# Optimization experiments

Hardware: AMD Instinct MI355X
Metric: run time of the kernel (lower is better)

Reference implementation:

```python
import jax, jax.numpy as jnp
import numpy as np

K = 27          # kernel volume = 3^3 (kernel_size=3, dimension=3)
M = 100000      # active in/out pairs per kernel offset
N_IN = 200000   # input sparse points
N_OUT = 400000  # output sparse points (stride-2 transpose upsample)
C_IN = 32
C_OUT = 32


def setup_inputs() -> dict:
    key = jax.random.key(0)
    k1, k2, k3, k4 = jax.random.split(key, 4)
    feats = jax.random.normal(k1, (N_IN, C_IN), dtype=jnp.float32)
    kernel = jax.random.normal(k2, (K, C_IN, C_OUT), dtype=jnp.float32) * 0.05
    in_map = jax.random.randint(k3, (K, M), 0, N_IN, dtype=jnp.int32)
    out_map = jax.random.randint(k4, (K, M), 0, N_OUT, dtype=jnp.int32)
    return {"feats": feats, "kernel": kernel, "in_map": in_map,
            "out_map": out_map, "n_out": N_OUT}


def reference(feats, kernel, in_map, out_map, n_out):
    # Sparse conv-transpose: for each kernel offset k,
    #   gather input rows, multiply by the offset's weight matrix,
    #   scatter-add into the output coordinate rows.
    gathered = feats[in_map]                              # [K, M, C_in]
    per_off = jnp.einsum('kmc,kcd->kmd', gathered, kernel)  # [K, M, C_out]
    c_out = kernel.shape[-1]
    out = jnp.zeros((n_out, c_out), dtype=feats.dtype)
    out = out.at[out_map.reshape(-1)].add(per_off.reshape(-1, c_out))
    return out
```

## Files before the change

### kernel.cpp

```cpp
#include <hip/hip_runtime.h>

#define KOFF 27
#define MPAIR 100000
#define NPAIR (KOFF * MPAIR)
#define NIN 200000
#define NOUT 400000
#define CIN 32
#define COUT 32

#define ROWS_PER_BIN 256
#define NBIN ((NOUT + ROWS_PER_BIN - 1) / ROWS_PER_BIN)
#define CAPB 3072
#define BPB 8192
#define SPILL_CAP 65536

#define O_SPCNT   ((size_t)8192)
#define O_SPILL   ((size_t)8448)
#define O_BINNED  ((size_t)532736)
#define O_PEROFF  ((size_t)19738880)
#define O_F16     ((size_t)192538880)
#define WS_NEED   ((size_t)205338880)

typedef unsigned int uint4n __attribute__((ext_vector_type(4)));

__device__ __forceinline__ unsigned int bf16pair(float a, float b) {
    unsigned int ua = __float_as_uint(a), ub = __float_as_uint(b);
    ua = (ua + 0x7fffu + ((ua >> 16) & 1u)) >> 16;
    ub = (ub + 0x7fffu + ((ub >> 16) & 1u)) >> 16;
    return ua | (ub << 16);
}
__device__ __forceinline__ float bf2f(unsigned short v) {
    return __uint_as_float(((unsigned int)v) << 16);
}
__device__ __forceinline__ float bf2f_lo(unsigned int w) {
    return __uint_as_float(w << 16);
}
__device__ __forceinline__ float bf2f_hi(unsigned int w) {
    return __uint_as_float(w & 0xFFFF0000u);
}

__global__ __launch_bounds__(256) void cvt_kernel(
    const float* __restrict__ feats, unsigned short* __restrict__ f16)
{
    int i = blockIdx.x * 256 + threadIdx.x;
    if (i >= NIN * CIN / 8) return;
    const float4* src = reinterpret_cast<const float4*>(feats) + i * 2;
    float4 a = src[0], b = src[1];
    uint4n u;
    u.x = bf16pair(a.x, a.y); u.y = bf16pair(a.z, a.w);
    u.z = bf16pair(b.x, b.y); u.w = bf16pair(b.z, b.w);
    reinterpret_cast<uint4n*>(f16)[i] = u;
}

__global__ __launch_bounds__(256) void bin_kernel(
    const int* __restrict__ out_map,
    int* __restrict__ gbin, int* __restrict__ binned,
    int* __restrict__ spill_cnt, int2* __restrict__ spill)
{
    __shared__ int lhist[NBIN];
    const int t = threadIdx.x;
    const int base = blockIdx.x * BPB;

    for (int c = t; c < NBIN; c += 256) lhist[c] = 0;
    __syncthreads();

    for (int i = t; i < BPB; i += 256) {
        int p = base + i;
        if (p < NPAIR) atomicAdd(&lhist[out_map[p] >> 8], 1);
    }
    __syncthreads();

    for (int c = t; c < NBIN; c += 256) {
        int cnt = lhist[c];
        lhist[c] = (cnt > 0) ? atomicAdd(&gbin[c], cnt) : 0;
    }
    __syncthreads();

    for (int i = t; i < BPB; i += 256) {
        int p = base + i;
        if (p >= NPAIR) continue;
        int row = out_map[p];
        int bin = row >> 8;
        int val = ((row & 255) << 22) | p;
        int pos = atomicAdd(&lhist[bin], 1);
        if (pos < CAPB) {
            binned[(size_t)bin * CAPB + pos] = val;
        } else {
            int o = atomicAdd(spill_cnt, 1);
            if (o < SPILL_CAP) spill[o] = make_int2(row, p);
        }
    }
}

__global__ __launch_bounds__(256) void mv_kernel(
    const unsigned short* __restrict__ f16, const float* __restrict__ weight,
    const int* __restrict__ in_map, unsigned short* __restrict__ per_off)
{
    const int k = blockIdx.y;
    const int m = blockIdx.x * 256 + threadIdx.x;
    if (m >= MPAIR) return;
    const int p = k * MPAIR + m;
    const int in_row = in_map[p];

    const uint4n* frow = reinterpret_cast<const uint4n*>(f16 + (size_t)in_row * CIN);
    uint4n q[2];
    q[0] = frow[0]; q[1] = frow[1];

    float f[CIN];
#pragma unroll
    for (int j = 0; j < 2; ++j) {
        f[j*16 + 0]  = bf2f_lo(q[j].x); f[j*16 + 1]  = bf2f_hi(q[j].x);
        f[j*16 + 2]  = bf2f_lo(q[j].y); f[j*16 + 3]  = bf2f_hi(q[j].y);
        f[j*16 + 4]  = bf2f_lo(q[j].z); f[j*16 + 5]  = bf2f_hi(q[j].z);
        f[j*16 + 6]  = bf2f_lo(q[j].w); f[j*16 + 7]  = bf2f_hi(q[j].w);
    }
    uint4n q2[2];
    q2[0] = frow[2]; q2[1] = frow[3];
#pragma unroll
    for (int j = 0; j < 2; ++j) {
        f[16 + j*8 + 0] = bf2f_lo(q2[j].x); f[16 + j*8 + 1] = bf2f_hi(q2[j].x);
        f[16 + j*8 + 2] = bf2f_lo(q2[j].y); f[16 + j*8 + 3] = bf2f_hi(q2[j].y);
        f[16 + j*8 + 4] = bf2f_lo(q2[j].z); f[16 + j*8 + 5] = bf2f_hi(q2[j].z);
        f[16 + j*8 + 6] = bf2f_lo(q2[j].w); f[16 + j*8 + 7] = bf2f_hi(q2[j].w);
    }
#pragma unroll
    for (int j = 0; j < 2; ++j) {
        f[j*8 + 0] = bf2f_lo(q[j].x); f[j*8 + 1] = bf2f_hi(q[j].x);
        f[j*8 + 2] = bf2f_lo(q[j].y); f[j*8 + 3] = bf2f_hi(q[j].y);
        f[j*8 + 4] = bf2f_lo(q[j].z); f[j*8 + 5] = bf2f_hi(q[j].z);
        f[j*8 + 6] = bf2f_lo(q[j].w); f[j*8 + 7] = bf2f_hi(q[j].w);
    }

    float acc[COUT];
#pragma unroll
    for (int i = 0; i < COUT; ++i) acc[i] = 0.f;

    const float* wk = weight + (size_t)k * (CIN * COUT);
#pragma unroll
    for (int ci = 0; ci < CIN; ++ci) {
        const float fv = f[ci];
#pragma unroll
        for (int co = 0; co < COUT; ++co)
            acc[co] = fmaf(fv, wk[ci * COUT + co], acc[co]);
    }

    uint4n u[4];
#pragma unroll
    for (int j = 0; j < 4; ++j) {
        u[j].x = bf16pair(acc[8 * j + 0], acc[8 * j + 1]);
        u[j].y = bf16pair(acc[8 * j + 2], acc[8 * j + 3]);
        u[j].z = bf16pair(acc[8 * j + 4], acc[8 * j + 5]);
        u[j].w = bf16pair(acc[8 * j + 6], acc[8 * j + 7]);
    }
    uint4n* dst = reinterpret_cast<uint4n*>(per_off + (size_t)p * COUT);
#pragma unroll
    for (int j = 0; j < 4; ++j) dst[j] = u[j];
}

__global__ __launch_bounds__(256) void gather3_kernel(
    const unsigned short* __restrict__ per_off,
    const int* __restrict__ gbin, const int* __restrict__ binned,
    float* __restrict__ out)
{
    __shared__ int sorted[CAPB];
    __shared__ int cnt[ROWS_PER_BIN];
    __shared__ int scn[ROWS_PER_BIN];
    __shared__ int cur[ROWS_PER_BIN];

    const int bin = blockIdx.x;
    const int t = threadIdx.x;
    const int n = min(gbin[bin], CAPB);
    const int* mybin = binned + (size_t)bin * CAPB;

    cnt[t] = 0;
    __syncthreads();

    for (int i = t; i < n; i += 256)
        atomicAdd(&cnt[(mybin[i] >> 22) & 255], 1);
    __syncthreads();

    scn[t] = cnt[t];
    __syncthreads();
#pragma unroll
    for (int off = 1; off < 256; off <<= 1) {
        int v = (t >= off) ? scn[t - off] : 0;
        __syncthreads();
        scn[t] += v;
        __syncthreads();
    }
    cur[t] = scn[t] - cnt[t];
    __syncthreads();

    for (int i = t; i < n; i += 256) {
        int v = mybin[i];
        int pos = atomicAdd(&cur[(v >> 22) & 255], 1);
        sorted[pos] = v & 0x3FFFFF;
    }
    __syncthreads();

    const int g = t >> 5, lane = t & 31;
    for (int r = g; r < ROWS_PER_BIN; r += 8) {
        int grow = (bin << 8) + r;
        if (grow >= NOUT) break;
        int s1 = scn[r], s0 = s1 - cnt[r];
        float a0 = 0.f, a1 = 0.f, a2 = 0.f, a3 = 0.f;
        int i = s0;
        for (; i + 4 <= s1; i += 4) {
            int p0 = sorted[i], p1 = sorted[i + 1], p2 = sorted[i + 2], p3 = sorted[i + 3];
            a0 += bf2f(per_off[(size_t)p0 * COUT + lane]);
            a1 += bf2f(per_off[(size_t)p1 * COUT + lane]);
            a2 += bf2f(per_off[(size_t)p2 * COUT + lane]);
            a3 += bf2f(per_off[(size_t)p3 * COUT + lane]);
        }
        for (; i < s1; ++i)
            a0 += bf2f(per_off[(size_t)sorted[i] * COUT + lane]);
        out[(size_t)grow * COUT + lane] = (a0 + a1) + (a2 + a3);
    }
}

__global__ __launch_bounds__(256) void spill_kernel(
    const float* __restrict__ feats, const float* __restrict__ weight,
    const int* __restrict__ in_map,
    const int* __restrict__ spill_cnt, const int2* __restrict__ spill,
    float* __restrict__ out)
{
    int n = min(*spill_cnt, SPILL_CAP);
    for (int i = blockIdx.x * blockDim.x + threadIdx.x; i < n * 32;
         i += gridDim.x * blockDim.x) {
        int idx = i >> 5, co = i & 31;
        int2 s = spill[idx];
        int row = s.x;
        int p   = s.y;
        int k   = p / MPAIR;
        int irow = in_map[p];
        const float* f  = feats + (size_t)irow * CIN;
        const float* wk = weight + (size_t)k * (CIN * COUT);
        float acc = 0.f;
#pragma unroll
        for (int ci = 0; ci < CIN; ++ci)
            acc = fmaf(f[ci], wk[ci * COUT + co], acc);
        atomicAdd(&out[(size_t)row * COUT + co], acc);
    }
}

__global__ __launch_bounds__(256) void spconvt_fallback(
    const float* __restrict__ feats, const float* __restrict__ weight,
    const int* __restrict__ in_map, const int* __restrict__ out_map,
    float* __restrict__ out)
{
    const int k = blockIdx.y;
    const int m = blockIdx.x * blockDim.x + threadIdx.x;
    const bool active = (m < MPAIR);
    const int mm = active ? m : (MPAIR - 1);
    const int pair = k * MPAIR + mm;
    const int in_row = in_map[pair];
    const int out_row = out_map[pair];
    const float4* frow = reinterpret_cast<const float4*>(feats + (size_t)in_row * CIN);
    float4 f4[8];
#pragma unroll
    for (int i = 0; i < 8; ++i) f4[i] = frow[i];
    const float* f = reinterpret_cast<const float*>(f4);
    float acc[COUT];
#pragma unroll
    for (int i = 0; i < COUT; ++i) acc[i] = 0.f;
    const float* wk = weight + (size_t)k * (CIN * COUT);
#pragma unroll
    for (int ci = 0; ci < CIN; ++ci) {
        const float fv = f[ci];
#pragma unroll
        for (int co = 0; co < COUT; ++co)
            acc[co] = fmaf(fv, wk[ci * COUT + co], acc[co]);
    }
    if (active) {
        float* orow = out + (size_t)out_row * COUT;
#pragma unroll
        for (int co = 0; co < COUT; ++co) atomicAdd(orow + co, acc[co]);
    }
}

extern "C" void kernel_launch(void* const* d_in, const int* in_sizes, int n_in,
                              void* d_out, int out_size, void* d_ws, size_t ws_size,
                              hipStream_t stream) {
    const float* feats  = (const float*)d_in[0];
    const float* weight = (const float*)d_in[1];
    const int* in_map   = (const int*)d_in[2];
    const int* out_map  = (const int*)d_in[3];
    float* out          = (float*)d_out;
    char* ws            = (char*)d_ws;

    if (ws_size >= WS_NEED) {
        int* gbin               = (int*)(ws);
        int* spill_cnt          = (int*)(ws + O_SPCNT);
        int2* spill             = (int2*)(ws + O_SPILL);
        int* binned             = (int*)(ws + O_BINNED);
        unsigned short* per_off = (unsigned short*)(ws + O_PEROFF);
        unsigned short* f16     = (unsigned short*)(ws + O_F16);

        (void)hipMemsetAsync(ws, 0, O_SPILL, stream);

        cvt_kernel<<<dim3((NIN * CIN / 8 + 255) / 256), dim3(256), 0, stream>>>(
            feats, f16);

        bin_kernel<<<dim3((NPAIR + BPB - 1) / BPB), dim3(256), 0, stream>>>(
            out_map, gbin, binned, spill_cnt, spill);

        mv_kernel<<<dim3((MPAIR + 255) / 256, KOFF), dim3(256), 0, stream>>>(
            f16, weight, in_map, per_off);

        gather3_kernel<<<dim3(NBIN), dim3(256), 0, stream>>>(
            per_off, gbin, binned, out);

        spill_kernel<<<dim3(64), dim3(256), 0, stream>>>(
            feats, weight, in_map, spill_cnt, spill, out);
    } else {
        (void)hipMemsetAsync(d_out, 0, (size_t)out_size * sizeof(float), stream);
        spconvt_fallback<<<dim3((MPAIR + 255) / 256, KOFF), dim3(256), 0, stream>>>(
            feats, weight, in_map, out_map, out);
    }
}
```

Baseline: 297.1 us.

## Counting-sort pairs by input-row chunk so the matvec gathers feats locally

Adds a three-pass counting sort (histogram, scan, scatter) that groups pairs by kernel offset and by 1024-row chunk of the input feature table. The matvec kernel is rewritten to walk each (offset, chunk) bucket, so the bf16 feature gathers hit a small, cache-resident region instead of random rows. This costs three extra passes over in_map plus a binned index buffer, and the per_off stores become scattered writes indexed by the original pair id. Blocks are ordered so the chunks of each offset group run together, which may help L2 reuse.

```diff
diff --git a/kernel.cpp b/kernel.cpp
--- a/kernel.cpp
+++ b/kernel.cpp
@@ -14,12 +14,20 @@
 #define BPB 8192
 #define SPILL_CAP 65536
 
-#define O_SPCNT   ((size_t)8192)
-#define O_SPILL   ((size_t)8448)
-#define O_BINNED  ((size_t)532736)
-#define O_PEROFF  ((size_t)19738880)
-#define O_F16     ((size_t)192538880)
-#define WS_NEED   ((size_t)205338880)
+#define CHROWS 1024
+#define NCHUNK ((NIN + CHROWS - 1) / CHROWS)
+#define NBINC (KOFF * NCHUNK)
+
+#define O_CNTC    ((size_t)8192)
+#define O_SPCNT   ((size_t)32768)
+#define O_SPILL   ((size_t)33024)
+#define O_BASC    ((size_t)560128)
+#define O_CURC    ((size_t)581632)
+#define O_BINNED  ((size_t)603136)
+#define O_BINI    ((size_t)19809280)
+#define O_PEROFF  ((size_t)30609280)
+#define O_F16     ((size_t)203409280)
+#define WS_NEED   ((size_t)216209280)
 
 typedef unsigned int uint4n __attribute__((ext_vector_type(4)));
 
@@ -50,6 +58,84 @@
     u.x = bf16pair(a.x, a.y); u.y = bf16pair(a.z, a.w);
     u.z = bf16pair(b.x, b.y); u.w = bf16pair(b.z, b.w);
     reinterpret_cast<uint4n*>(f16)[i] = u;
+}
+
+__global__ __launch_bounds__(256) void histc_kernel(
+    const int* __restrict__ in_map, int* __restrict__ cntc)
+{
+    __shared__ int h[NBINC];
+    const int t = threadIdx.x;
+    const int base = blockIdx.x * BPB;
+    for (int c = t; c < NBINC; c += 256) h[c] = 0;
+    __syncthreads();
+    for (int i = t; i < BPB; i += 256) {
+        int p = base + i;
+        if (p < NPAIR) {
+            int key = (p / MPAIR) * NCHUNK + (in_map[p] >> 10);
+            atomicAdd(&h[key], 1);
+        }
+    }
+    __syncthreads();
+    for (int c = t; c < NBINC; c += 256) if (h[c]) atomicAdd(&cntc[c], h[c]);
+}
+
+__global__ __launch_bounds__(256) void scanc_kernel(
+    const int* __restrict__ cntc, int* __restrict__ basc, int* __restrict__ curc)
+{
+    __shared__ int lsum[256];
+    const int t = threadIdx.x;
+    int v[21]; int s = 0;
+#pragma unroll
+    for (int j = 0; j < 21; ++j) {
+        int i = t * 21 + j;
+        v[j] = (i < NBINC) ? cntc[i] : 0;
+        s += v[j];
+    }
+    lsum[t] = s;
+    __syncthreads();
+    for (int off = 1; off < 256; off <<= 1) {
+        int w = (t >= off) ? lsum[t - off] : 0;
+        __syncthreads();
+        lsum[t] += w;
+        __syncthreads();
+    }
+    int run = lsum[t] - s;
+#pragma unroll
+    for (int j = 0; j < 21; ++j) {
+        int i = t * 21 + j;
+        if (i < NBINC) { basc[i] = run; curc[i] = run; run += v[j]; }
+    }
+    if (t == 255) basc[NBINC] = run;
+}
+
+__global__ __launch_bounds__(256) void scatc_kernel(
+    const int* __restrict__ in_map, int* __restrict__ curc,
+    unsigned int* __restrict__ binned_in)
+{
+    __shared__ int h[NBINC];
+    const int t = threadIdx.x;
+    const int base = blockIdx.x * BPB;
+    for (int c = t; c < NBINC; c += 256) h[c] = 0;
+    __syncthreads();
+    for (int i = t; i < BPB; i += 256) {
+        int p = base + i;
+        if (p < NPAIR)
+            atomicAdd(&h[(p / MPAIR) * NCHUNK + (in_map[p] >> 10)], 1);
+    }
+    __syncthreads();
+    for (int c = t; c < NBINC; c += 256) {
+        int v = h[c];
+        h[c] = v ? atomicAdd(&curc[c], v) : 0;
+    }
+    __syncthreads();
+    for (int i = t; i < BPB; i += 256) {
+        int p = base + i;
+        if (p >= NPAIR) continue;
+        int ir = in_map[p];
+        int key = (p / MPAIR) * NCHUNK + (ir >> 10);
+        int slot = atomicAdd(&h[key], 1);
+        binned_in[slot] = ((unsigned int)(ir & 1023) << 22) | (unsigned int)p;
+    }
 }
 
 __global__ __launch_bounds__(256) void bin_kernel(
@@ -92,69 +178,77 @@
     }
 }
 
-__global__ __launch_bounds__(256) void mv_kernel(
+__global__ __launch_bounds__(256) void mv3_kernel(
     const unsigned short* __restrict__ f16, const float* __restrict__ weight,
-    const int* __restrict__ in_map, unsigned short* __restrict__ per_off)
-{
-    const int k = blockIdx.y;
-    const int m = blockIdx.x * 256 + threadIdx.x;
-    if (m >= MPAIR) return;
-    const int p = k * MPAIR + m;
-    const int in_row = in_map[p];
-
-    const uint4n* frow = reinterpret_cast<const uint4n*>(f16 + (size_t)in_row * CIN);
-    uint4n q[2];
-    q[0] = frow[0]; q[1] = frow[1];
-
-    float f[CIN];
-#pragma unroll
-    for (int j = 0; j < 2; ++j) {
-        f[j*16 + 0]  = bf2f_lo(q[j].x); f[j*16 + 1]  = bf2f_hi(q[j].x);
-        f[j*16 + 2]  = bf2f_lo(q[j].y); f[j*16 + 3]  = bf2f_hi(q[j].y);
-        f[j*16 + 4]  = bf2f_lo(q[j].z); f[j*16 + 5]  = bf2f_hi(q[j].z);
-        f[j*16 + 6]  = bf2f_lo(q[j].w); f[j*16 + 7]  = bf2f_hi(q[j].w);
-    }
-    uint4n q2[2];
-    q2[0] = frow[2]; q2[1] = frow[3];
-#pragma unroll
-    for (int j = 0; j < 2; ++j) {
-        f[16 + j*8 + 0] = bf2f_lo(q2[j].x); f[16 + j*8 + 1] = bf2f_hi(q2[j].x);
-        f[16 + j*8 + 2] = bf2f_lo(q2[j].y); f[16 + j*8 + 3] = bf2f_hi(q2[j].y);
-        f[16 + j*8 + 4] = bf2f_lo(q2[j].z); f[16 + j*8 + 5] = bf2f_hi(q2[j].z);
-        f[16 + j*8 + 6] = bf2f_lo(q2[j].w); f[16 + j*8 + 7] = bf2f_hi(q2[j].w);
-    }
-#pragma unroll
-    for (int j = 0; j < 2; ++j) {
-        f[j*8 + 0] = bf2f_lo(q[j].x); f[j*8 + 1] = bf2f_hi(q[j].x);
-        f[j*8 + 2] = bf2f_lo(q[j].y); f[j*8 + 3] = bf2f_hi(q[j].y);
-        f[j*8 + 4] = bf2f_lo(q[j].z); f[j*8 + 5] = bf2f_hi(q[j].z);
-        f[j*8 + 6] = bf2f_lo(q[j].w); f[j*8 + 7] = bf2f_hi(q[j].w);
-    }
-
-    float acc[COUT];
-#pragma unroll
-    for (int i = 0; i < COUT; ++i) acc[i] = 0.f;
+    const int* __restrict__ basc, const unsigned int* __restrict__ binned_in,
+    unsigned short* __restrict__ per_off)
+{
+    int g = blockIdx.x;
+    int k, chunk;
+    if (g < 24 * 216) {
+        int grp = g / 216, rem = g % 216;
+        k = rem >> 3;
+        chunk = grp * 8 + (rem & 7);
+    } else {
+        int tl = g - 24 * 216;
+        k = tl >> 2;
+        chunk = 192 + (tl & 3);
+    }
+    const int key = k * NCHUNK + chunk;
+    const int s0 = basc[key], s1 = basc[key + 1];
+    const int t = threadIdx.x;
 
     const float* wk = weight + (size_t)k * (CIN * COUT);
-#pragma unroll
-    for (int ci = 0; ci < CIN; ++ci) {
-        const float fv = f[ci];
-#pragma unroll
-        for (int co = 0; co < COUT; ++co)
-            acc[co] = fmaf(fv, wk[ci * COUT + co], acc[co]);
-    }
-
-    uint4n u[4];
-#pragma unroll
-    for (int j = 0; j < 4; ++j) {
-        u[j].x = bf16pair(acc[8 * j + 0], acc[8 * j + 1]);
-        u[j].y = bf16pair(acc[8 * j + 2], acc[8 * j + 3]);
-        u[j].z = bf16pair(acc[8 * j + 4], acc[8 * j + 5]);
-        u[j].w = bf16pair(acc[8 * j + 6], acc[8 * j + 7]);
-    }
-    uint4n* dst = reinterpret_cast<uint4n*>(per_off + (size_t)p * COUT);
-#pragma unroll
-    for (int j = 0; j < 4; ++j) dst[j] = u[j];
+
+    for (int i = s0 + t; i < s1; i += 256) {
+        unsigned int e = binned_in[i];
+        int rl = (int)(e >> 22);
+        int p  = (int)(e & 0x3FFFFFu);
+        int row = (chunk << 10) + rl;
+
+        const uint4n* frow = reinterpret_cast<const uint4n*>(f16 + (size_t)row * CIN);
+        uint4n q0 = frow[0], q1 = frow[1], q2 = frow[2], q3 = frow[3];
+
+        float f[CIN];
+        f[0] = bf2f_lo(q0.x);  f[1] = bf2f_hi(q0.x);
+        f[2] = bf2f_lo(q0.y);  f[3] = bf2f_hi(q0.y);
+        f[4] = bf2f_lo(q0.z);  f[5] = bf2f_hi(q0.z);
+        f[6] = bf2f_lo(q0.w);  f[7] = bf2f_hi(q0.w);
+        f[8] = bf2f_lo(q1.x);  f[9] = bf2f_hi(q1.x);
+        f[10] = bf2f_lo(q1.y); f[11] = bf2f_hi(q1.y);
+        f[12] = bf2f_lo(q1.z); f[13] = bf2f_hi(q1.z);
+        f[14] = bf2f_lo(q1.w); f[15] = bf2f_hi(q1.w);
+        f[16] = bf2f_lo(q2.x); f[17] = bf2f_hi(q2.x);
+        f[18] = bf2f_lo(q2.y); f[19] = bf2f_hi(q2.y);
+        f[20] = bf2f_lo(q2.z); f[21] = bf2f_hi(q2.z);
+        f[22] = bf2f_lo(q2.w); f[23] = bf2f_hi(q2.w);
+        f[24] = bf2f_lo(q3.x); f[25] = bf2f_hi(q3.x);
+        f[26] = bf2f_lo(q3.y); f[27] = bf2f_hi(q3.y);
+        f[28] = bf2f_lo(q3.z); f[29] = bf2f_hi(q3.z);
+        f[30] = bf2f_lo(q3.w); f[31] = bf2f_hi(q3.w);
+
+        float acc[COUT];
+#pragma unroll
+        for (int j = 0; j < COUT; ++j) acc[j] = 0.f;
+#pragma unroll
+        for (int ci = 0; ci < CIN; ++ci) {
+            float fv = f[ci];
+#pragma unroll
+            for (int co = 0; co < COUT; ++co)
+                acc[co] = fmaf(fv, wk[ci * COUT + co], acc[co]);
+        }
+
+        uint4n u;
+        uint4n* dst = reinterpret_cast<uint4n*>(per_off + (size_t)p * COUT);
+#pragma unroll
+        for (int j = 0; j < 4; ++j) {
+            u.x = bf16pair(acc[8 * j + 0], acc[8 * j + 1]);
+            u.y = bf16pair(acc[8 * j + 2], acc[8 * j + 3]);
+            u.z = bf16pair(acc[8 * j + 4], acc[8 * j + 5]);
+            u.w = bf16pair(acc[8 * j + 6], acc[8 * j + 7]);
+            dst[j] = u;
+        }
+    }
 }
 
 __global__ __launch_bounds__(256) void gather3_kernel(
@@ -290,9 +384,13 @@
 
     if (ws_size >= WS_NEED) {
         int* gbin               = (int*)(ws);
+        int* cntc               = (int*)(ws + O_CNTC);
         int* spill_cnt          = (int*)(ws + O_SPCNT);
         int2* spill             = (int2*)(ws + O_SPILL);
+        int* basc               = (int*)(ws + O_BASC);
+        int* curc               = (int*)(ws + O_CURC);
         int* binned             = (int*)(ws + O_BINNED);
+        unsigned int* binned_in = (unsigned int*)(ws + O_BINI);
         unsigned short* per_off = (unsigned short*)(ws + O_PEROFF);
         unsigned short* f16     = (unsigned short*)(ws + O_F16);
 
@@ -301,11 +399,17 @@
         cvt_kernel<<<dim3((NIN * CIN / 8 + 255) / 256), dim3(256), 0, stream>>>(
             feats, f16);
 
+        histc_kernel<<<dim3((NPAIR + BPB - 1) / BPB), dim3(256), 0, stream>>>(
+            in_map, cntc);
+        scanc_kernel<<<dim3(1), dim3(256), 0, stream>>>(cntc, basc, curc);
+        scatc_kernel<<<dim3((NPAIR + BPB - 1) / BPB), dim3(256), 0, stream>>>(
+            in_map, curc, binned_in);
+
         bin_kernel<<<dim3((NPAIR + BPB - 1) / BPB), dim3(256), 0, stream>>>(
             out_map, gbin, binned, spill_cnt, spill);
 
-        mv_kernel<<<dim3((MPAIR + 255) / 256, KOFF), dim3(256), 0, stream>>>(
-            f16, weight, in_map, per_off);
+        mv3_kernel<<<dim3(NBINC), dim3(256), 0, stream>>>(
+            f16, weight, basc, binned_in, per_off);
 
         gather3_kernel<<<dim3(NBIN), dim3(256), 0, stream>>>(
             per_off, gbin, binned, out);
```

Result: slower. 652.4 us (+119.6%).
